# Optimization experiments

Hardware: AMD Instinct MI355X
Metric: run time of the kernel (lower is better)

Reference implementation:

```python
import jax, jax.numpy as jnp
import numpy as np

B, L, D = 2, 2048, 1024
K, M = 32, 4
H = D // K
AH = 4            # anchor heads
DH = K - AH       # decay heads
CK = 4            # conv kernel size
TOTAL = 2 * D + K + K * M


def setup_inputs() -> dict:
    key = jax.random.key(0)
    ks = jax.random.split(key, 7)
    x = jax.random.normal(ks[0], (B, L, D), jnp.float32)
    mask = jnp.ones((B, L), jnp.float32)
    W_in = jax.random.normal(ks[1], (D, TOTAL), jnp.float32) * 0.02
    conv_w = jax.random.normal(ks[2], (CK, TOTAL), jnp.float32) * 0.1  # depthwise taps
    conv_b = jnp.zeros((TOTAL,), jnp.float32)
    grid = np.linspace(-np.pi / 3, np.pi / 3, M).astype(np.float32)
    theta_base = jnp.asarray(np.tile(grid.reshape(1, 1, 1, 1, M), (1, 1, K, 1, 1)))
    theta_resid_scale = jnp.full((K,), 0.1, jnp.float32)
    dr = np.geomspace(0.001, 0.1, DH).astype(np.float32)
    decay_slopes = jnp.asarray(np.log(np.exp(dr) - 1.0).astype(np.float32))
    ar = np.geomspace(0.01, 0.1, AH).astype(np.float32)
    anchor_slopes = jnp.asarray(np.log(np.exp(ar) - 1.0).astype(np.float32))
    score_scale = jnp.ones((K,), jnp.float32)
    norm_scale = jnp.ones((2 * H * M,), jnp.float32)
    gl = float((2.0 / (H * M + H)) ** 0.5)  # glorot std
    W_re = jax.random.normal(ks[3], (H * M, H), jnp.float32) * gl
    W_im = jax.random.normal(ks[4], (H * M, H), jnp.float32) * gl
    W_out = jax.random.normal(ks[5], (D, D), jnp.float32) * 0.02
    return dict(x=x, mask=mask, W_in=W_in, conv_w=conv_w, conv_b=conv_b,
                theta_base=theta_base, theta_resid_scale=theta_resid_scale,
                decay_slopes=decay_slopes, anchor_slopes=anchor_slopes,
                score_scale=score_scale, norm_scale=norm_scale,
                W_re=W_re, W_im=W_im, W_out=W_out)


def _forward(x, mask, W_in, conv_w, conv_b, theta_base, theta_resid_scale,
             decay_slopes, anchor_slopes, score_scale, norm_scale, W_re, W_im, W_out):
    b, l, d = x.shape
    z = x @ W_in  # (b,l,TOTAL)
    # causal depthwise conv, kernel size CK
    zp = jnp.pad(z, ((0, 0), (CK - 1, 0), (0, 0)))
    z = sum(zp[:, t:t + l, :] * conv_w[t] for t in range(CK)) + conv_b

    x_val = z[..., :D].reshape(b, l, K, H)
    x_gate = jax.nn.silu(z[..., D:2 * D])
    s_raw = z[..., 2 * D:2 * D + K].reshape(b, l, K, 1)
    theta_raw = z[..., 2 * D + K:].reshape(b, l, K, M)

    theta_delta = theta_raw / (1.0 + jnp.abs(theta_raw))
    theta_dyn = theta_base + theta_resid_scale.reshape(1, 1, K, 1, 1) * (
        theta_delta.reshape(b, l, K, 1, M) * jnp.float32(np.pi / 3))

    m = mask[:, :, None, None]
    s_raw = s_raw * m
    x_val = x_val * m

    pos = jnp.arange(l, dtype=jnp.float32)
    slopes_d = jax.nn.softplus(decay_slopes).reshape(1, 1, DH, 1)
    dist_d = jnp.maximum(jnp.float32(l - 1) - pos, 0.0)[None, :, None, None]
    w_decay = jnp.exp(-slopes_d * dist_d)
    slopes_a = jax.nn.softplus(anchor_slopes).reshape(1, 1, AH, 1)
    w_anchor = jnp.exp(-slopes_a * pos[None, :, None, None])
    time_weight = jnp.concatenate([w_decay, w_anchor], axis=2)  # (1,l,K,1)

    p = jnp.exp(jnp.clip(score_scale[None, None, :, None] * s_raw, -20.0, 20.0))
    p = p * m

    phi = x_val[..., None] * theta_dyn  # (b,l,K,H,M)
    cos_b = jnp.cos(phi)
    sin_b = jnp.sin(phi)
    p_w = (p * time_weight)[..., None]  # (b,l,K,1,1)

    flat = (b, l, K * H * M)
    merged = jnp.concatenate([
        (p_w * cos_b).reshape(flat),
        (p_w * sin_b).reshape(flat),
        jnp.broadcast_to(p_w, (b, l, K, H, M)).reshape(flat)], axis=-1)
    cs = jnp.cumsum(merged, axis=1)
    num_re, num_im, den = jnp.split(cs, 3, axis=-1)
    inv_den = 1.0 / jnp.maximum(den, jnp.float32(1e-4))
    re = (num_re * inv_den).reshape(b, l, K, H * M)
    im = (num_im * inv_den).reshape(b, l, K, H * M)

    mean_sq = (jnp.sum(re * re, axis=-1) + jnp.sum(im * im, axis=-1)) * (1.0 / (2.0 * H * M))
    rsq = jax.lax.rsqrt(mean_sq[..., None] + 1e-5)
    y = (re * rsq * norm_scale[:H * M]) @ W_re + (im * rsq * norm_scale[H * M:]) @ W_im  # (b,l,K,H)
    y = y.reshape(b, l, D)
    return (y * x_gate) @ W_out


def reference(x, mask, W_in, conv_w, conv_b, theta_base, theta_resid_scale,
              decay_slopes, anchor_slopes, score_scale, norm_scale, W_re, W_im, W_out):
    return _forward(x, mask, W_in, conv_w, conv_b, theta_base, theta_resid_scale,
                    decay_slopes, anchor_slopes, score_scale, norm_scale, W_re, W_im, W_out)
```

## Files before the change

### kernel.cpp

```cpp
#include <hip/hip_runtime.h>
#include <hip/hip_bf16.h>
#include <math.h>

#define B_ 2
#define L_ 2048
#define D_ 1024
#define K_ 32
#define M_ 4
#define H_ 32
#define AH_ 4
#define DH_ 28
#define CK_ 4
#define TOTAL_ 2208
#define NPAD_ 2304
#define BL_ (B_*L_)
#define CL_ 16
#define NC_ (L_/CL_)
#define CTS_ 280
#define ZS_ 72

typedef __attribute__((ext_vector_type(8))) short bf16x8;
typedef __attribute__((ext_vector_type(4))) float f32x4;

static __device__ inline unsigned short f2bu(float f) {
    union { __hip_bfloat16 h; unsigned short u; } cv;
    cv.h = __float2bfloat16(f);
    return cv.u;
}
static __device__ inline float b2f(unsigned short u) {
    union { unsigned short u; __hip_bfloat16 h; } cv;
    cv.u = u;
    return __bfloat162float(cv.h);
}

__global__ void convert_x(const float4* __restrict__ src, ushort* __restrict__ dst) {
    int i = blockIdx.x * 256 + threadIdx.x;
    float4 v = src[i];
    ushort4 o;
    o.x = f2bu(v.x); o.y = f2bu(v.y); o.z = f2bu(v.z); o.w = f2bu(v.w);
    *(ushort4*)(dst + (size_t)i * 4) = o;
}

__global__ void transpose_bf16_pad(const float* __restrict__ src, ushort* __restrict__ dst,
                                   int K, int N) {
    __shared__ float tile[64][65];
    int n0 = blockIdx.x * 64, k0 = blockIdx.y * 64;
    int t = threadIdx.x;
#pragma unroll
    for (int i = 0; i < 16; ++i) {
        int idx = t + i * 256;
        int r = idx >> 6, c = idx & 63;
        int gn = n0 + c;
        tile[r][c] = (gn < N) ? src[(size_t)(k0 + r) * N + gn] : 0.f;
    }
    __syncthreads();
#pragma unroll
    for (int i = 0; i < 16; ++i) {
        int idx = t + i * 256;
        int r = idx >> 6, c = idx & 63;
        dst[(size_t)(n0 + r) * K + k0 + c] = f2bu(tile[c][r]);
    }
}

__global__ void prep_w2(const float* __restrict__ Wre, const float* __restrict__ Wim,
                        const float* __restrict__ nscale, ushort* __restrict__ W2B) {
    int ch = threadIdx.x;
    float ns = nscale[ch];
    for (int hout = 0; hout < 32; ++hout) {
        float w = (ch < 128) ? Wre[ch * 32 + hout] : Wim[(ch - 128) * 32 + hout];
        W2B[hout * 256 + ch] = f2bu(ns * w);
    }
}

__global__ __launch_bounds__(256) void gemm_bt(const ushort* __restrict__ A,
                                               const ushort* __restrict__ Bt,
                                               float* __restrict__ C,
                                               int Kd, int ldc) {
    __shared__ __align__(16) ushort As[128 * 32];
    __shared__ __align__(16) ushort Bs[128 * 32];
    int tid = threadIdx.x;
    int wave = tid >> 6, lane = tid & 63;
    int quad = lane >> 4, l16 = lane & 15;
    int m0 = blockIdx.y * 128, n0 = blockIdx.x * 128;
    int wm = (wave >> 1) * 64, wn = (wave & 1) * 64;
    f32x4 acc[4][4];
#pragma unroll
    for (int i = 0; i < 4; ++i)
#pragma unroll
        for (int j = 0; j < 4; ++j) acc[i][j] = (f32x4){0.f, 0.f, 0.f, 0.f};

    int swzq = quad ^ (l16 & 3);

    for (int k0 = 0; k0 < Kd; k0 += 32) {
#pragma unroll
        for (int i = 0; i < 2; ++i) {
            int s = i * 256 + tid;
            int row = s >> 2;
            int qg = (s & 3) ^ (row & 3);
            const ushort* ga = A + (size_t)(m0 + row) * Kd + k0 + qg * 8;
            const ushort* gb = Bt + (size_t)(n0 + row) * Kd + k0 + qg * 8;
            __builtin_amdgcn_global_load_lds((const __attribute__((address_space(1))) void*)ga,
                                             (__attribute__((address_space(3))) void*)(As + (size_t)s * 8),
                                             16, 0, 0);
            __builtin_amdgcn_global_load_lds((const __attribute__((address_space(1))) void*)gb,
                                             (__attribute__((address_space(3))) void*)(Bs + (size_t)s * 8),
                                             16, 0, 0);
        }
        __syncthreads();
        bf16x8 af[4], bfr[4];
#pragma unroll
        for (int mi = 0; mi < 4; ++mi)
            af[mi] = *(const bf16x8*)(As + (size_t)(wm + mi * 16 + l16) * 32 + swzq * 8);
#pragma unroll
        for (int ni = 0; ni < 4; ++ni)
            bfr[ni] = *(const bf16x8*)(Bs + (size_t)(wn + ni * 16 + l16) * 32 + swzq * 8);
#pragma unroll
        for (int mi = 0; mi < 4; ++mi)
#pragma unroll
            for (int ni = 0; ni < 4; ++ni)
                acc[mi][ni] = __builtin_amdgcn_mfma_f32_16x16x32_bf16(af[mi], bfr[ni], acc[mi][ni], 0, 0, 0);
        __syncthreads();
    }
#pragma unroll
    for (int mi = 0; mi < 4; ++mi)
#pragma unroll
        for (int ni = 0; ni < 4; ++ni)
#pragma unroll
            for (int r = 0; r < 4; ++r) {
                int gm = m0 + wm + mi * 16 + quad * 4 + r;
                int gn = n0 + wn + ni * 16 + l16;
                C[(size_t)gm * ldc + gn] = acc[mi][ni][r];
            }
}

__global__ void conv_kernel(const float* __restrict__ z, const float* __restrict__ cw,
                            const float* __restrict__ cb, float* __restrict__ zck) {
    int t = blockIdx.x * 256 + threadIdx.x;
    if (t >= BL_ * (TOTAL_ / 4)) return;
    int c4 = (t % (TOTAL_ / 4)) * 4;
    int bl = t / (TOTAL_ / 4);
    int l = bl % L_, b = bl / L_;
    float4 acc = *(const float4*)(cb + c4);
#pragma unroll
    for (int tap = 0; tap < CK_; ++tap) {
        int ls = l - (CK_ - 1) + tap;
        if (ls >= 0) {
            float4 zv = *(const float4*)(z + (size_t)(bl - (CK_ - 1) + tap) * NPAD_ + c4);
            float4 wv = *(const float4*)(cw + tap * TOTAL_ + c4);
            acc.x = fmaf(zv.x, wv.x, acc.x);
            acc.y = fmaf(zv.y, wv.y, acc.y);
            acc.z = fmaf(zv.z, wv.z, acc.z);
            acc.w = fmaf(zv.w, wv.w, acc.w);
        }
    }
    if (c4 < D_) {
        int k = c4 >> 5, slot = c4 & 31;
        *(float4*)(zck + ((size_t)(b * K_ + k) * L_ + l) * ZS_ + slot) = acc;
    } else if (c4 < 2 * D_) {
        int cc = c4 - D_;
        int k = cc >> 5, slot = 32 + (cc & 31);
        *(float4*)(zck + ((size_t)(b * K_ + k) * L_ + l) * ZS_ + slot) = acc;
    } else if (c4 < 2 * D_ + K_) {
        float av[4] = {acc.x, acc.y, acc.z, acc.w};
#pragma unroll
        for (int q = 0; q < 4; ++q) {
            int k = c4 + q - 2 * D_;
            zck[((size_t)(b * K_ + k) * L_ + l) * ZS_ + 64] = av[q];
        }
    } else {
        int j = c4 - (2 * D_ + K_);
        int k = j >> 2;
        *(float4*)(zck + ((size_t)(b * K_ + k) * L_ + l) * ZS_ + 68) = acc;
    }
}

__global__ __launch_bounds__(128) void pass1(const float* __restrict__ zck,
                                             const float* __restrict__ mask,
                                             const float* __restrict__ theta_base,
                                             const float* __restrict__ trs_,
                                             const float* __restrict__ dslopes,
                                             const float* __restrict__ aslopes,
                                             const float* __restrict__ sscale_,
                                             const ushort* __restrict__ W2B,
                                             float* __restrict__ cs_re,
                                             float* __restrict__ cs_im,
                                             float* __restrict__ cs_den,
                                             float* __restrict__ vc) {
    __shared__ __align__(16) ushort ct[CL_ * CTS_];
    int nc = blockIdx.x, k = blockIdx.y, b = blockIdx.z;
    int hm = threadIdx.x;
    int h = hm >> 2, m = hm & 3;
    int bk = b * K_ + k;
    size_t bkL = (size_t)bk * L_;
    float raw = (k < DH_) ? dslopes[k] : aslopes[k - DH_];
    float slope = log1pf(__expf(raw));
    float sscale = sscale_[k];
    float trsv = trs_[k];
    float tb = theta_base[k * M_ + m];
    const float PI3 = 1.04719755119659775f;
    float are = 0.f, aim = 0.f, aden = 0.f;
    int l0 = nc * CL_;
#pragma unroll 4
    for (int i = 0; i < CL_; ++i) {
        int l = l0 + i;
        const float* zrow = zck + (bkL + l) * ZS_;
        float mval = mask[b * L_ + l];
        float s_raw = zrow[64] * mval;
        float tr = zrow[68 + m];
        float xv = zrow[h] * mval;
        float arg = fminf(fmaxf(sscale * s_raw, -20.f), 20.f);
        float p = __expf(arg) * mval;
        float tw = (k < DH_) ? __expf(-slope * (float)(L_ - 1 - l)) : __expf(-slope * (float)l);
        float pw = p * tw;
        float td = tr / (1.f + fabsf(tr));
        float theta = tb + trsv * (td * PI3);
        float phi = xv * theta;
        float sv = __sinf(phi), cv = __cosf(phi);
        unsigned short cu_re = f2bu(pw * cv);
        unsigned short cu_im = f2bu(pw * sv);
        are += b2f(cu_re); aim += b2f(cu_im); aden += pw;
        ct[i * CTS_ + hm] = cu_re;
        ct[i * CTS_ + 128 + hm] = cu_im;
    }
    size_t o = ((size_t)(bk * NC_ + nc)) * 128 + hm;
    cs_re[o] = are;
    cs_im[o] = aim;
    if (hm == 0) cs_den[bk * NC_ + nc] = aden;
    __syncthreads();
    int wave = hm >> 6, lane = hm & 63;
    int quad = lane >> 4, l16 = lane & 15;
    f32x4 acc = (f32x4){0.f, 0.f, 0.f, 0.f};
#pragma unroll
    for (int ks = 0; ks < 8; ++ks) {
        bf16x8 af = *(const bf16x8*)(ct + (size_t)l16 * CTS_ + ks * 32 + quad * 8);
        bf16x8 bfr = *(const bf16x8*)(W2B + (size_t)(wave * 16 + l16) * 256 + ks * 32 + quad * 8);
        acc = __builtin_amdgcn_mfma_f32_16x16x32_bf16(af, bfr, acc, 0, 0, 0);
    }
    size_t vbase = (bkL + l0) * 32;
#pragma unroll
    for (int r = 0; r < 4; ++r) {
        int row = quad * 4 + r;
        vc[vbase + (size_t)row * 32 + wave * 16 + l16] = acc[r];
    }
}

__global__ void pass2(float* cs_re, float* cs_im, float* cs_den) {
    int seq = blockIdx.x * 256 + threadIdx.x;
    if (seq >= B_ * K_ * 257) return;
    int bk = seq / 257;
    int ch = seq % 257;
    float* base;
    int stride;
    if (ch < 128) { base = cs_re + (size_t)bk * NC_ * 128 + ch; stride = 128; }
    else if (ch < 256) { base = cs_im + (size_t)bk * NC_ * 128 + (ch - 128); stride = 128; }
    else { base = cs_den + (size_t)bk * NC_; stride = 1; }
    float run = 0.f;
#pragma unroll 4
    for (int i = 0; i < NC_; ++i) {
        float v = base[(size_t)i * stride];
        base[(size_t)i * stride] = run;
        run += v;
    }
}

__global__ __launch_bounds__(64) void scan_kernel(const float* __restrict__ zck,
                                                  const float* __restrict__ mask,
                                                  const float* __restrict__ theta_base,
                                                  const float* __restrict__ trs_,
                                                  const float* __restrict__ dslopes,
                                                  const float* __restrict__ aslopes,
                                                  const float* __restrict__ sscale_,
                                                  const ushort* __restrict__ W2B,
                                                  const float* __restrict__ cs_re,
                                                  const float* __restrict__ cs_im,
                                                  const float* __restrict__ cs_den,
                                                  const float* __restrict__ vc,
                                                  ushort* __restrict__ gq) {
    int nc = blockIdx.x, k = blockIdx.y, b = blockIdx.z;
    int lane = threadIdx.x;
    int bk = b * K_ + k;
    size_t bkL = (size_t)bk * L_;
    int h0 = lane >> 2, h1 = 16 + (lane >> 2), m = lane & 3;
    int hout = lane & 31, half = lane >> 5;
    float raw = (k < DH_) ? dslopes[k] : aslopes[k - DH_];
    float slope = log1pf(__expf(raw));
    float sscale = sscale_[k];
    float trsv = trs_[k];
    float tb = theta_base[k * M_ + m];
    const float PI3 = 1.04719755119659775f;

    size_t o = ((size_t)(bk * NC_ + nc)) * 128;
    const float* srcp = half ? (cs_im + o) : (cs_re + o);
    float u = 0.f;
#pragma unroll 8
    for (int i = 0; i < 128; ++i)
        u = fmaf(srcp[i], b2f(W2B[hout * 256 + half * 128 + i]), u);
    u += __shfl_xor(u, 32, 64);

    float are0 = cs_re[o + lane];
    float are1 = cs_re[o + 64 + lane];
    float aim0 = cs_im[o + lane];
    float aim1 = cs_im[o + 64 + lane];
    float den = cs_den[bk * NC_ + nc];
    int l0 = nc * CL_;

#pragma unroll 4
    for (int i = 0; i < CL_; ++i) {
        int l = l0 + i;
        const float* zrow = zck + (bkL + l) * ZS_;
        float mval = mask[b * L_ + l];
        float s_raw = zrow[64] * mval;
        float tr = zrow[68 + m];
        float xv0 = zrow[h0] * mval;
        float xv1 = zrow[h1] * mval;
        float arg = fminf(fmaxf(sscale * s_raw, -20.f), 20.f);
        float p = __expf(arg) * mval;
        float tw = (k < DH_) ? __expf(-slope * (float)(L_ - 1 - l)) : __expf(-slope * (float)l);
        float pw = p * tw;
        float td = tr / (1.f + fabsf(tr));
        float theta = tb + trsv * (td * PI3);
        float s0 = __sinf(xv0 * theta), c0 = __cosf(xv0 * theta);
        float s1 = __sinf(xv1 * theta), c1 = __cosf(xv1 * theta);
        float cre0 = b2f(f2bu(pw * c0)), cim0 = b2f(f2bu(pw * s0));
        float cre1 = b2f(f2bu(pw * c1)), cim1 = b2f(f2bu(pw * s1));
        are0 += cre0; aim0 += cim0; are1 += cre1; aim1 += cim1;
        den += pw;
        float s = are0 * are0 + are1 * are1 + aim0 * aim0 + aim1 * aim1;
#pragma unroll
        for (int off = 32; off; off >>= 1) s += __shfl_xor(s, off, 64);
        float inv = 1.f / fmaxf(den, 1e-4f);
        float rsq = rsqrtf(inv * inv * s * (1.0f / 256.0f) + 1e-5f);
        float scv = inv * rsq;
        u += vc[(bkL + l) * 32 + hout];
        float y = scv * u;
        float zg = zrow[32 + hout];
        float gate = zg / (1.f + __expf(-zg));
        if (lane < 32) gq[(size_t)(b * L_ + l) * D_ + k * H_ + hout] = f2bu(y * gate);
    }
}

extern "C" void kernel_launch(void* const* d_in, const int* in_sizes, int n_in,
                              void* d_out, int out_size, void* d_ws, size_t ws_size,
                              hipStream_t stream) {
    const float* x = (const float*)d_in[0];
    const float* mask = (const float*)d_in[1];
    const float* W_in = (const float*)d_in[2];
    const float* conv_w = (const float*)d_in[3];
    const float* conv_b = (const float*)d_in[4];
    const float* theta_base = (const float*)d_in[5];
    const float* trs = (const float*)d_in[6];
    const float* dsl = (const float*)d_in[7];
    const float* asl = (const float*)d_in[8];
    const float* ssc = (const float*)d_in[9];
    const float* nsc = (const float*)d_in[10];
    const float* Wre = (const float*)d_in[11];
    const float* Wim = (const float*)d_in[12];
    const float* Wout = (const float*)d_in[13];
    float* out = (float*)d_out;

    char* ws = (char*)d_ws;
    float* zck = (float*)(ws);
    float* z      = (float*)(ws + 37748736ULL);
    float* cs_re  = (float*)(ws + 37748736ULL);
    float* cs_im  = (float*)(ws + 41943040ULL);
    float* cs_den = (float*)(ws + 46137344ULL);
    ushort* gq    = (ushort*)(ws + 46170112ULL);
    ushort* x_bf  = (ushort*)(ws + 75497472ULL);
    ushort* Wt_in = (ushort*)(ws + 83886080ULL);
    float* vc     = (float*)(ws + 75497472ULL);
    ushort* Wt_o  = (ushort*)(ws + 92274688ULL);
    ushort* W2B   = (ushort*)(ws + 94371840ULL);

    convert_x<<<4096, 256, 0, stream>>>((const float4*)x, x_bf);
    transpose_bf16_pad<<<dim3(NPAD_ / 64, 16), 256, 0, stream>>>(W_in, Wt_in, 1024, TOTAL_);
    transpose_bf16_pad<<<dim3(16, 16), 256, 0, stream>>>(Wout, Wt_o, 1024, 1024);
    prep_w2<<<1, 256, 0, stream>>>(Wre, Wim, nsc, W2B);
    gemm_bt<<<dim3(NPAD_ / 128, BL_ / 128), 256, 0, stream>>>(x_bf, Wt_in, z, 1024, NPAD_);
    conv_kernel<<<(BL_ * (TOTAL_ / 4) + 255) / 256, 256, 0, stream>>>(z, conv_w, conv_b, zck);
    pass1<<<dim3(NC_, K_, B_), 128, 0, stream>>>(zck, mask, theta_base, trs, dsl, asl, ssc,
                                                 W2B, cs_re, cs_im, cs_den, vc);
    pass2<<<(B_ * K_ * 257 + 255) / 256, 256, 0, stream>>>(cs_re, cs_im, cs_den);
    scan_kernel<<<dim3(NC_, K_, B_), 64, 0, stream>>>(zck, mask, theta_base, trs, dsl, asl, ssc,
                                                      W2B, cs_re, cs_im, cs_den, vc, gq);
    gemm_bt<<<dim3(D_ / 128, BL_ / 128), 256, 0, stream>>>(gq, Wt_o, out, 1024, 1024);
}
```

Baseline: 304.1 us.

## Cache pass1 contributions and scan projected outputs instead of recomputing in scan

Adds a new path, taken when the workspace is large enough. The conv kernel writes per-head rows with the silu gate precomputed in bf16. pass1 stores its bf16 contributions and time-weighted scores, and new kernels build a prefix sum of the projected vc values, so the final scan no longer recomputes sin/cos or runs the MFMA projection per step. This trades recomputation for more global memory traffic and extra kernel launches, and the path only runs if ws_size meets the new threshold.

```diff
diff --git a/kernel.cpp b/kernel.cpp
--- a/kernel.cpp
+++ b/kernel.cpp
@@ -18,6 +18,7 @@
 #define NC_ (L_/CL_)
 #define CTS_ 280
 #define ZS_ 72
+#define ZS2_ 128
 
 typedef __attribute__((ext_vector_type(8))) short bf16x8;
 typedef __attribute__((ext_vector_type(4))) float f32x4;
@@ -132,6 +133,213 @@
                 C[(size_t)gm * ldc + gn] = acc[mi][ni][r];
             }
 }
+
+
+__global__ void conv_fast(const float* __restrict__ z, const float* __restrict__ cw,
+                          const float* __restrict__ cb, float* __restrict__ zck2,
+                          ushort* __restrict__ gateb) {
+    int t = blockIdx.x * 256 + threadIdx.x;
+    if (t >= BL_ * (TOTAL_ / 4)) return;
+    int c4 = (t % (TOTAL_ / 4)) * 4;
+    int bl = t / (TOTAL_ / 4);
+    int l = bl % L_, b = bl / L_;
+    float4 acc = *(const float4*)(cb + c4);
+#pragma unroll
+    for (int tap = 0; tap < CK_; ++tap) {
+        int ls = l - (CK_ - 1) + tap;
+        if (ls >= 0) {
+            float4 zv = *(const float4*)(z + (size_t)(bl - (CK_ - 1) + tap) * NPAD_ + c4);
+            float4 wv = *(const float4*)(cw + tap * TOTAL_ + c4);
+            acc.x = fmaf(zv.x, wv.x, acc.x);
+            acc.y = fmaf(zv.y, wv.y, acc.y);
+            acc.z = fmaf(zv.z, wv.z, acc.z);
+            acc.w = fmaf(zv.w, wv.w, acc.w);
+        }
+    }
+    if (c4 < D_) {
+        int k = c4 >> 5, slot = c4 & 31;
+        *(float4*)(zck2 + ((size_t)(b * K_ + k) * L_ + l) * ZS2_ + slot) = acc;
+    } else if (c4 < 2 * D_) {
+        int cc = c4 - D_;
+        int k = cc >> 5, hh = cc & 31;
+        float av[4] = {acc.x, acc.y, acc.z, acc.w};
+        ushort4 o;
+        unsigned short* op = (unsigned short*)&o;
+#pragma unroll
+        for (int q = 0; q < 4; ++q) {
+            float zg = av[q];
+            op[q] = f2bu(zg / (1.f + __expf(-zg)));
+        }
+        *(ushort4*)(gateb + ((size_t)(b * K_ + k) * L_ + l) * 32 + hh) = o;
+    } else if (c4 < 2 * D_ + K_) {
+        float av[4] = {acc.x, acc.y, acc.z, acc.w};
+#pragma unroll
+        for (int q = 0; q < 4; ++q) {
+            int k = c4 + q - 2 * D_;
+            zck2[((size_t)(b * K_ + k) * L_ + l) * ZS2_ + 32] = av[q];
+        }
+    } else {
+        int j = c4 - (2 * D_ + K_);
+        int k = j >> 2;
+        *(float4*)(zck2 + ((size_t)(b * K_ + k) * L_ + l) * ZS2_ + 36) = acc;
+    }
+}
+
+__global__ __launch_bounds__(128) void pass1_fast(const float* zck2,
+                                                  const float* __restrict__ mask,
+                                                  const float* __restrict__ theta_base,
+                                                  const float* __restrict__ trs_,
+                                                  const float* __restrict__ dslopes,
+                                                  const float* __restrict__ aslopes,
+                                                  const float* __restrict__ sscale_,
+                                                  const ushort* __restrict__ W2B,
+                                                  float* __restrict__ cs_re,
+                                                  float* __restrict__ cs_im,
+                                                  float* __restrict__ cs_den,
+                                                  float* __restrict__ vc,
+                                                  ushort* ctb,
+                                                  float* __restrict__ pwb) {
+    __shared__ __align__(16) ushort ct[CL_ * CTS_];
+    int nc = blockIdx.x, k = blockIdx.y, b = blockIdx.z;
+    int hm = threadIdx.x;
+    int h = hm >> 2, m = hm & 3;
+    int bk = b * K_ + k;
+    size_t bkL = (size_t)bk * L_;
+    float raw = (k < DH_) ? dslopes[k] : aslopes[k - DH_];
+    float slope = log1pf(__expf(raw));
+    float sscale = sscale_[k];
+    float trsv = trs_[k];
+    float tb = theta_base[k * M_ + m];
+    const float PI3 = 1.04719755119659775f;
+    float are = 0.f, aim = 0.f, aden = 0.f;
+    int l0 = nc * CL_;
+    float tw = (k < DH_) ? __expf(-slope * (float)(L_ - 1 - l0)) : __expf(-slope * (float)l0);
+    float e_s = (k < DH_) ? __expf(slope) : __expf(-slope);
+#pragma unroll 4
+    for (int i = 0; i < CL_; ++i) {
+        int l = l0 + i;
+        const float* zrow = zck2 + (bkL + l) * ZS2_;
+        float mval = mask[b * L_ + l];
+        float s_raw = zrow[32] * mval;
+        float tr = zrow[36 + m];
+        float xv = zrow[h] * mval;
+        float arg = fminf(fmaxf(sscale * s_raw, -20.f), 20.f);
+        float p = __expf(arg) * mval;
+        float pw = p * tw;
+        float td = tr / (1.f + fabsf(tr));
+        float theta = tb + trsv * (td * PI3);
+        float phi = xv * theta;
+        float sv = __sinf(phi), cv = __cosf(phi);
+        unsigned short cu_re = f2bu(pw * cv);
+        unsigned short cu_im = f2bu(pw * sv);
+        are += b2f(cu_re); aim += b2f(cu_im); aden += pw;
+        ct[i * CTS_ + hm] = cu_re;
+        ct[i * CTS_ + 128 + hm] = cu_im;
+        if (hm == 0) pwb[bkL + l] = pw;
+        tw *= e_s;
+    }
+    size_t o = ((size_t)(bk * NC_ + nc)) * 128 + hm;
+    cs_re[o] = are;
+    cs_im[o] = aim;
+    if (hm == 0) cs_den[bk * NC_ + nc] = aden;
+    __syncthreads();
+    int wave = hm >> 6, lane = hm & 63;
+    int quad = lane >> 4, l16 = lane & 15;
+    f32x4 acc = (f32x4){0.f, 0.f, 0.f, 0.f};
+#pragma unroll
+    for (int ks = 0; ks < 8; ++ks) {
+        bf16x8 af = *(const bf16x8*)(ct + (size_t)l16 * CTS_ + ks * 32 + quad * 8);
+        bf16x8 bfr = *(const bf16x8*)(W2B + (size_t)(wave * 16 + l16) * 256 + ks * 32 + quad * 8);
+        acc = __builtin_amdgcn_mfma_f32_16x16x32_bf16(af, bfr, acc, 0, 0, 0);
+    }
+    size_t vbase = (bkL + l0) * 32;
+#pragma unroll
+    for (int r = 0; r < 4; ++r) {
+        int row = quad * 4 + r;
+        vc[vbase + (size_t)row * 32 + wave * 16 + l16] = acc[r];
+    }
+#pragma unroll
+    for (int t = hm; t < CL_ * 64; t += 128) {
+        int i = t >> 6, ln = t & 63;
+        ushort4 w;
+        w.x = ct[i * CTS_ + ln];
+        w.y = ct[i * CTS_ + 64 + ln];
+        w.z = ct[i * CTS_ + 128 + ln];
+        w.w = ct[i * CTS_ + 192 + ln];
+        *(ushort4*)(ctb + (bkL + l0 + i) * 256 + ln * 4) = w;
+    }
+}
+
+__global__ void ucs_kernel(const float* __restrict__ vc, float* __restrict__ ucs) {
+    int idx = blockIdx.x * 256 + threadIdx.x;
+    int hout = idx & 31;
+    int nc = (idx >> 5) & (NC_ - 1);
+    int bk = idx >> 12;
+    float s = 0.f;
+#pragma unroll
+    for (int j = 0; j < CL_; ++j)
+        s += vc[(((size_t)bk * L_) + nc * CL_ + j) * 32 + hout];
+    ucs[((size_t)bk * NC_ + nc) * 32 + hout] = s;
+}
+
+__global__ void uscan_kernel(const float* __restrict__ ucs, float* __restrict__ u_prev) {
+    int idx = blockIdx.x * 256 + threadIdx.x;
+    if (idx >= 64 * 32) return;
+    int hout = idx & 31;
+    int bk = idx >> 5;
+    float run = 0.f;
+#pragma unroll 8
+    for (int nc = 0; nc < NC_; ++nc) {
+        size_t o = ((size_t)bk * NC_ + nc) * 32 + hout;
+        float v = ucs[o];
+        u_prev[o] = run;
+        run += v;
+    }
+}
+
+__global__ __launch_bounds__(64) void scan_fast(const ushort* __restrict__ ctb,
+                                                const float* __restrict__ pwb,
+                                                const float* __restrict__ cs_re,
+                                                const float* __restrict__ cs_im,
+                                                const float* __restrict__ cs_den,
+                                                const float* __restrict__ u_prev,
+                                                const float* __restrict__ vc,
+                                                const ushort* __restrict__ gateb,
+                                                ushort* __restrict__ gq) {
+    int nc = blockIdx.x, k = blockIdx.y, b = blockIdx.z;
+    int lane = threadIdx.x;
+    int bk = b * K_ + k;
+    size_t bkL = (size_t)bk * L_;
+    int hout = lane & 31;
+
+    size_t o = ((size_t)(bk * NC_ + nc)) * 128;
+    float are0 = cs_re[o + lane];
+    float are1 = cs_re[o + 64 + lane];
+    float aim0 = cs_im[o + lane];
+    float aim1 = cs_im[o + 64 + lane];
+    float den = cs_den[bk * NC_ + nc];
+    float u = u_prev[((size_t)(bk * NC_ + nc)) * 32 + hout];
+    int l0 = nc * CL_;
+
+#pragma unroll 4
+    for (int i = 0; i < CL_; ++i) {
+        int l = l0 + i;
+        ushort4 cb = *(const ushort4*)(ctb + (bkL + l) * 256 + lane * 4);
+        float pw = pwb[bkL + l];
+        are0 += b2f(cb.x); are1 += b2f(cb.y);
+        aim0 += b2f(cb.z); aim1 += b2f(cb.w);
+        den += pw;
+        float s = are0 * are0 + are1 * are1 + aim0 * aim0 + aim1 * aim1;
+#pragma unroll
+        for (int off = 32; off; off >>= 1) s += __shfl_xor(s, off, 64);
+        float inv = 1.f / fmaxf(den, 1e-4f);
+        float rsq = rsqrtf(inv * inv * s * (1.0f / 256.0f) + 1e-5f);
+        u += vc[(bkL + l) * 32 + hout];
+        float gv = inv * rsq * u * b2f(gateb[(bkL + l) * 32 + hout]);
+        if (lane < 32) gq[(size_t)(b * L_ + l) * D_ + k * H_ + hout] = f2bu(gv);
+    }
+}
+
 
 __global__ void conv_kernel(const float* __restrict__ z, const float* __restrict__ cw,
                             const float* __restrict__ cb, float* __restrict__ zck) {
@@ -359,28 +567,64 @@
     float* out = (float*)d_out;
 
     char* ws = (char*)d_ws;
-    float* zck = (float*)(ws);
-    float* z      = (float*)(ws + 37748736ULL);
-    float* cs_re  = (float*)(ws + 37748736ULL);
-    float* cs_im  = (float*)(ws + 41943040ULL);
-    float* cs_den = (float*)(ws + 46137344ULL);
-    ushort* gq    = (ushort*)(ws + 46170112ULL);
-    ushort* x_bf  = (ushort*)(ws + 75497472ULL);
-    ushort* Wt_in = (ushort*)(ws + 83886080ULL);
-    float* vc     = (float*)(ws + 75497472ULL);
-    ushort* Wt_o  = (ushort*)(ws + 92274688ULL);
-    ushort* W2B   = (ushort*)(ws + 94371840ULL);
-
-    convert_x<<<4096, 256, 0, stream>>>((const float4*)x, x_bf);
-    transpose_bf16_pad<<<dim3(NPAD_ / 64, 16), 256, 0, stream>>>(W_in, Wt_in, 1024, TOTAL_);
-    transpose_bf16_pad<<<dim3(16, 16), 256, 0, stream>>>(Wout, Wt_o, 1024, 1024);
-    prep_w2<<<1, 256, 0, stream>>>(Wre, Wim, nsc, W2B);
-    gemm_bt<<<dim3(NPAD_ / 128, BL_ / 128), 256, 0, stream>>>(x_bf, Wt_in, z, 1024, NPAD_);
-    conv_kernel<<<(BL_ * (TOTAL_ / 4) + 255) / 256, 256, 0, stream>>>(z, conv_w, conv_b, zck);
-    pass1<<<dim3(NC_, K_, B_), 128, 0, stream>>>(zck, mask, theta_base, trs, dsl, asl, ssc,
-                                                 W2B, cs_re, cs_im, cs_den, vc);
-    pass2<<<(B_ * K_ * 257 + 255) / 256, 256, 0, stream>>>(cs_re, cs_im, cs_den);
-    scan_kernel<<<dim3(NC_, K_, B_), 64, 0, stream>>>(zck, mask, theta_base, trs, dsl, asl, ssc,
-                                                      W2B, cs_re, cs_im, cs_den, vc, gq);
-    gemm_bt<<<dim3(D_ / 128, BL_ / 128), 256, 0, stream>>>(gq, Wt_o, out, 1024, 1024);
-}
+    const size_t NEED_FAST = 115359744ULL;
+
+    if (ws_size >= NEED_FAST) {
+        float* zck2   = (float*)(ws);
+        ushort* ctb   = (ushort*)(ws);
+        ushort* x_bf  = (ushort*)(ws);
+        ushort* Wt_in = (ushort*)(ws + 8388608ULL);
+        ushort* gateb = (ushort*)(ws + 67108864ULL);
+        float* z      = (float*)(ws + 75497472ULL);
+        float* vc     = (float*)(ws + 75497472ULL);
+        float* cs_re  = (float*)(ws + 92274688ULL);
+        float* cs_im  = (float*)(ws + 96468992ULL);
+        float* cs_den = (float*)(ws + 100663296ULL);
+        float* pwb    = (float*)(ws + 100696064ULL);
+        float* u_prev = (float*)(ws + 101220352ULL);
+        float* ucs    = (float*)(ws + 102268928ULL);
+        ushort* gq    = (ushort*)(ws + 103317504ULL);
+        ushort* Wt_o  = (ushort*)(ws + 113246208ULL);
+        ushort* W2B   = (ushort*)(ws + 115343360ULL);
+
+        convert_x<<<4096, 256, 0, stream>>>((const float4*)x, x_bf);
+        transpose_bf16_pad<<<dim3(NPAD_ / 64, 16), 256, 0, stream>>>(W_in, Wt_in, 1024, TOTAL_);
+        transpose_bf16_pad<<<dim3(16, 16), 256, 0, stream>>>(Wout, Wt_o, 1024, 1024);
+        prep_w2<<<1, 256, 0, stream>>>(Wre, Wim, nsc, W2B);
+        gemm_bt<<<dim3(NPAD_ / 128, BL_ / 128), 256, 0, stream>>>(x_bf, Wt_in, z, 1024, NPAD_);
+        conv_fast<<<(BL_ * (TOTAL_ / 4) + 255) / 256, 256, 0, stream>>>(z, conv_w, conv_b, zck2, gateb);
+        pass1_fast<<<dim3(NC_, K_, B_), 128, 0, stream>>>(zck2, mask, theta_base, trs, dsl, asl,
+                                                          ssc, W2B, cs_re, cs_im, cs_den, vc, ctb, pwb);
+        pass2<<<(B_ * K_ * 257 + 255) / 256, 256, 0, stream>>>(cs_re, cs_im, cs_den);
+        ucs_kernel<<<1024, 256, 0, stream>>>(vc, ucs);
+        uscan_kernel<<<8, 256, 0, stream>>>(ucs, u_prev);
+        scan_fast<<<dim3(NC_, K_, B_), 64, 0, stream>>>(ctb, pwb, cs_re, cs_im, cs_den,
+                                                        u_prev, vc, gateb, gq);
+        gemm_bt<<<dim3(D_ / 128, BL_ / 128), 256, 0, stream>>>(gq, Wt_o, out, 1024, 1024);
+    } else {
+        float* zck    = (float*)(ws);
+        float* z      = (float*)(ws + 37748736ULL);
+        float* cs_re  = (float*)(ws + 37748736ULL);
+        float* cs_im  = (float*)(ws + 41943040ULL);
+        float* cs_den = (float*)(ws + 46137344ULL);
+        ushort* gq    = (ushort*)(ws + 46170112ULL);
+        ushort* x_bf  = (ushort*)(ws + 75497472ULL);
+        ushort* Wt_in = (ushort*)(ws + 83886080ULL);
+        float* vc     = (float*)(ws + 75497472ULL);
+        ushort* Wt_o  = (ushort*)(ws + 92274688ULL);
+        ushort* W2B   = (ushort*)(ws + 94371840ULL);
+
+        convert_x<<<4096, 256, 0, stream>>>((const float4*)x, x_bf);
+        transpose_bf16_pad<<<dim3(NPAD_ / 64, 16), 256, 0, stream>>>(W_in, Wt_in, 1024, TOTAL_);
+        transpose_bf16_pad<<<dim3(16, 16), 256, 0, stream>>>(Wout, Wt_o, 1024, 1024);
+        prep_w2<<<1, 256, 0, stream>>>(Wre, Wim, nsc, W2B);
+        gemm_bt<<<dim3(NPAD_ / 128, BL_ / 128), 256, 0, stream>>>(x_bf, Wt_in, z, 1024, NPAD_);
+        conv_kernel<<<(BL_ * (TOTAL_ / 4) + 255) / 256, 256, 0, stream>>>(z, conv_w, conv_b, zck);
+        pass1<<<dim3(NC_, K_, B_), 128, 0, stream>>>(zck, mask, theta_base, trs, dsl, asl, ssc,
+                                                     W2B, cs_re, cs_im, cs_den, vc);
+        pass2<<<(B_ * K_ * 257 + 255) / 256, 256, 0, stream>>>(cs_re, cs_im, cs_den);
+        scan_kernel<<<dim3(NC_, K_, B_), 64, 0, stream>>>(zck, mask, theta_base, trs, dsl, asl, ssc,
+                                                          W2B, cs_re, cs_im, cs_den, vc, gq);
+        gemm_bt<<<dim3(D_ / 128, BL_ / 128), 256, 0, stream>>>(gq, Wt_o, out, 1024, 1024);
+    }
+}
```

After: 301.1 us. No clear change (-1.0%).

## Fuse causal conv into scan passes, merge prep kernels, scan chunk u-offsets

Applied to the files above, without the earlier changes.

Removes the standalone conv kernel and the reshaped zck buffer. The depthwise causal conv is recomputed inside pass1 and the scan kernel from raw z, using register sliding windows. The four prep kernels are merged into one launch. The time-weight exp is replaced by a running multiply. The scan kernel's per-chunk 128-wide dot product for the u offset is replaced by per-chunk partial sums written in pass1 and prefix-scanned in the combined scan2 kernel. This saves a full write and read of the intermediate and several launches, at the cost of strided uncoalesced z reads (row stride NPAD) in the scan kernels and some redundant conv work.

```diff
diff --git a/kernel.cpp b/kernel.cpp
--- a/kernel.cpp
+++ b/kernel.cpp
@@ -17,7 +17,6 @@
 #define CL_ 16
 #define NC_ (L_/CL_)
 #define CTS_ 280
-#define ZS_ 72
 
 typedef __attribute__((ext_vector_type(8))) short bf16x8;
 typedef __attribute__((ext_vector_type(4))) float f32x4;
@@ -32,20 +31,49 @@
     cv.u = u;
     return __bfloat162float(cv.h);
 }
-
-__global__ void convert_x(const float4* __restrict__ src, ushort* __restrict__ dst) {
-    int i = blockIdx.x * 256 + threadIdx.x;
-    float4 v = src[i];
-    ushort4 o;
-    o.x = f2bu(v.x); o.y = f2bu(v.y); o.z = f2bu(v.z); o.w = f2bu(v.w);
-    *(ushort4*)(dst + (size_t)i * 4) = o;
-}
-
-__global__ void transpose_bf16_pad(const float* __restrict__ src, ushort* __restrict__ dst,
-                                   int K, int N) {
+static __device__ inline float conv4(float bias, const float w[4], float r0, float r1,
+                                     float r2, float zc) {
+    return fmaf(w[3], zc, fmaf(w[2], r2, fmaf(w[1], r1, fmaf(w[0], r0, bias))));
+}
+
+__global__ __launch_bounds__(256) void prep_all(const float* __restrict__ x,
+                                                const float* __restrict__ W_in,
+                                                const float* __restrict__ Wout,
+                                                const float* __restrict__ Wre,
+                                                const float* __restrict__ Wim,
+                                                const float* __restrict__ nscale,
+                                                ushort* __restrict__ x_bf,
+                                                ushort* __restrict__ Wt_in,
+                                                ushort* __restrict__ Wt_o,
+                                                ushort* __restrict__ W2B) {
     __shared__ float tile[64][65];
-    int n0 = blockIdx.x * 64, k0 = blockIdx.y * 64;
-    int t = threadIdx.x;
+    int bid = blockIdx.x, t = threadIdx.x;
+    if (bid < 4096) {
+        int i = bid * 256 + t;
+        float4 v = ((const float4*)x)[i];
+        ushort4 o;
+        o.x = f2bu(v.x); o.y = f2bu(v.y); o.z = f2bu(v.z); o.w = f2bu(v.w);
+        *(ushort4*)(x_bf + (size_t)i * 4) = o;
+        return;
+    }
+    const float* src; ushort* dst; int Kd, N, n0, k0;
+    if (bid < 4096 + 576) {
+        int bb = bid - 4096;
+        src = W_in; dst = Wt_in; Kd = 1024; N = TOTAL_;
+        n0 = (bb % 36) * 64; k0 = (bb / 36) * 64;
+    } else if (bid < 4096 + 576 + 256) {
+        int bb = bid - 4096 - 576;
+        src = Wout; dst = Wt_o; Kd = 1024; N = 1024;
+        n0 = (bb % 16) * 64; k0 = (bb / 16) * 64;
+    } else {
+        int ch = t;
+        float ns = nscale[ch];
+        for (int ho = 0; ho < 32; ++ho) {
+            float w = (ch < 128) ? Wre[ch * 32 + ho] : Wim[(ch - 128) * 32 + ho];
+            W2B[ho * 256 + ch] = f2bu(ns * w);
+        }
+        return;
+    }
 #pragma unroll
     for (int i = 0; i < 16; ++i) {
         int idx = t + i * 256;
@@ -58,17 +86,7 @@
     for (int i = 0; i < 16; ++i) {
         int idx = t + i * 256;
         int r = idx >> 6, c = idx & 63;
-        dst[(size_t)(n0 + r) * K + k0 + c] = f2bu(tile[c][r]);
-    }
-}
-
-__global__ void prep_w2(const float* __restrict__ Wre, const float* __restrict__ Wim,
-                        const float* __restrict__ nscale, ushort* __restrict__ W2B) {
-    int ch = threadIdx.x;
-    float ns = nscale[ch];
-    for (int hout = 0; hout < 32; ++hout) {
-        float w = (ch < 128) ? Wre[ch * 32 + hout] : Wim[(ch - 128) * 32 + hout];
-        W2B[hout * 256 + ch] = f2bu(ns * w);
+        dst[(size_t)(n0 + r) * Kd + k0 + c] = f2bu(tile[c][r]);
     }
 }
 
@@ -133,85 +151,70 @@
             }
 }
 
-__global__ void conv_kernel(const float* __restrict__ z, const float* __restrict__ cw,
-                            const float* __restrict__ cb, float* __restrict__ zck) {
-    int t = blockIdx.x * 256 + threadIdx.x;
-    if (t >= BL_ * (TOTAL_ / 4)) return;
-    int c4 = (t % (TOTAL_ / 4)) * 4;
-    int bl = t / (TOTAL_ / 4);
-    int l = bl % L_, b = bl / L_;
-    float4 acc = *(const float4*)(cb + c4);
-#pragma unroll
-    for (int tap = 0; tap < CK_; ++tap) {
-        int ls = l - (CK_ - 1) + tap;
-        if (ls >= 0) {
-            float4 zv = *(const float4*)(z + (size_t)(bl - (CK_ - 1) + tap) * NPAD_ + c4);
-            float4 wv = *(const float4*)(cw + tap * TOTAL_ + c4);
-            acc.x = fmaf(zv.x, wv.x, acc.x);
-            acc.y = fmaf(zv.y, wv.y, acc.y);
-            acc.z = fmaf(zv.z, wv.z, acc.z);
-            acc.w = fmaf(zv.w, wv.w, acc.w);
-        }
-    }
-    if (c4 < D_) {
-        int k = c4 >> 5, slot = c4 & 31;
-        *(float4*)(zck + ((size_t)(b * K_ + k) * L_ + l) * ZS_ + slot) = acc;
-    } else if (c4 < 2 * D_) {
-        int cc = c4 - D_;
-        int k = cc >> 5, slot = 32 + (cc & 31);
-        *(float4*)(zck + ((size_t)(b * K_ + k) * L_ + l) * ZS_ + slot) = acc;
-    } else if (c4 < 2 * D_ + K_) {
-        float av[4] = {acc.x, acc.y, acc.z, acc.w};
-#pragma unroll
-        for (int q = 0; q < 4; ++q) {
-            int k = c4 + q - 2 * D_;
-            zck[((size_t)(b * K_ + k) * L_ + l) * ZS_ + 64] = av[q];
-        }
-    } else {
-        int j = c4 - (2 * D_ + K_);
-        int k = j >> 2;
-        *(float4*)(zck + ((size_t)(b * K_ + k) * L_ + l) * ZS_ + 68) = acc;
-    }
-}
-
-__global__ __launch_bounds__(128) void pass1(const float* __restrict__ zck,
-                                             const float* __restrict__ mask,
-                                             const float* __restrict__ theta_base,
-                                             const float* __restrict__ trs_,
-                                             const float* __restrict__ dslopes,
-                                             const float* __restrict__ aslopes,
-                                             const float* __restrict__ sscale_,
-                                             const ushort* __restrict__ W2B,
-                                             float* __restrict__ cs_re,
-                                             float* __restrict__ cs_im,
-                                             float* __restrict__ cs_den,
-                                             float* __restrict__ vc) {
+__global__ __launch_bounds__(128) void pass1f(const float* __restrict__ z,
+                                              const float* __restrict__ mask,
+                                              const float* __restrict__ theta_base,
+                                              const float* __restrict__ trs_,
+                                              const float* __restrict__ dslopes,
+                                              const float* __restrict__ aslopes,
+                                              const float* __restrict__ sscale_,
+                                              const float* __restrict__ conv_w,
+                                              const float* __restrict__ conv_b,
+                                              const ushort* __restrict__ W2B,
+                                              float* __restrict__ cs_re,
+                                              float* __restrict__ cs_im,
+                                              float* __restrict__ cs_den,
+                                              float* __restrict__ vc,
+                                              float* __restrict__ ucs) {
     __shared__ __align__(16) ushort ct[CL_ * CTS_];
     int nc = blockIdx.x, k = blockIdx.y, b = blockIdx.z;
     int hm = threadIdx.x;
     int h = hm >> 2, m = hm & 3;
     int bk = b * K_ + k;
     size_t bkL = (size_t)bk * L_;
+    int cxv = k * H_ + h, csc = 2 * D_ + k, cth = 2 * D_ + K_ + k * M_ + m;
+    float wx[4], ws4[4], wt4[4];
+#pragma unroll
+    for (int t = 0; t < 4; ++t) {
+        wx[t] = conv_w[t * TOTAL_ + cxv];
+        ws4[t] = conv_w[t * TOTAL_ + csc];
+        wt4[t] = conv_w[t * TOTAL_ + cth];
+    }
+    float bx = conv_b[cxv], bs = conv_b[csc], bt = conv_b[cth];
+    int l0 = nc * CL_;
+    float rx[3], rs[3], rt[3];
+#pragma unroll
+    for (int j = 0; j < 3; ++j) {
+        int ls = l0 - 3 + j;
+        if (ls >= 0) {
+            size_t zo = (size_t)(b * L_ + ls) * NPAD_;
+            rx[j] = z[zo + cxv]; rs[j] = z[zo + csc]; rt[j] = z[zo + cth];
+        } else { rx[j] = 0.f; rs[j] = 0.f; rt[j] = 0.f; }
+    }
     float raw = (k < DH_) ? dslopes[k] : aslopes[k - DH_];
     float slope = log1pf(__expf(raw));
-    float sscale = sscale_[k];
-    float trsv = trs_[k];
-    float tb = theta_base[k * M_ + m];
+    float sscale = sscale_[k], trsv = trs_[k], tb = theta_base[k * M_ + m];
     const float PI3 = 1.04719755119659775f;
+    float tw = (k < DH_) ? __expf(-slope * (float)(L_ - 1 - l0)) : __expf(-slope * (float)l0);
+    float e_s = (k < DH_) ? __expf(slope) : __expf(-slope);
     float are = 0.f, aim = 0.f, aden = 0.f;
-    int l0 = nc * CL_;
 #pragma unroll 4
     for (int i = 0; i < CL_; ++i) {
         int l = l0 + i;
-        const float* zrow = zck + (bkL + l) * ZS_;
-        float mval = mask[b * L_ + l];
-        float s_raw = zrow[64] * mval;
-        float tr = zrow[68 + m];
-        float xv = zrow[h] * mval;
+        int row = b * L_ + l;
+        size_t zo = (size_t)row * NPAD_;
+        float zx = z[zo + cxv], zs = z[zo + csc], zt = z[zo + cth];
+        float mval = mask[row];
+        float xv = conv4(bx, wx, rx[0], rx[1], rx[2], zx) * mval;
+        float s_raw = conv4(bs, ws4, rs[0], rs[1], rs[2], zs) * mval;
+        float tr = conv4(bt, wt4, rt[0], rt[1], rt[2], zt);
+        rx[0] = rx[1]; rx[1] = rx[2]; rx[2] = zx;
+        rs[0] = rs[1]; rs[1] = rs[2]; rs[2] = zs;
+        rt[0] = rt[1]; rt[1] = rt[2]; rt[2] = zt;
         float arg = fminf(fmaxf(sscale * s_raw, -20.f), 20.f);
         float p = __expf(arg) * mval;
-        float tw = (k < DH_) ? __expf(-slope * (float)(L_ - 1 - l)) : __expf(-slope * (float)l);
         float pw = p * tw;
+        tw *= e_s;
         float td = tr / (1.f + fabsf(tr));
         float theta = tb + trsv * (td * PI3);
         float phi = xv * theta;
@@ -239,90 +242,137 @@
     size_t vbase = (bkL + l0) * 32;
 #pragma unroll
     for (int r = 0; r < 4; ++r) {
-        int row = quad * 4 + r;
-        vc[vbase + (size_t)row * 32 + wave * 16 + l16] = acc[r];
-    }
-}
-
-__global__ void pass2(float* cs_re, float* cs_im, float* cs_den) {
-    int seq = blockIdx.x * 256 + threadIdx.x;
-    if (seq >= B_ * K_ * 257) return;
-    int bk = seq / 257;
-    int ch = seq % 257;
-    float* base;
-    int stride;
-    if (ch < 128) { base = cs_re + (size_t)bk * NC_ * 128 + ch; stride = 128; }
-    else if (ch < 256) { base = cs_im + (size_t)bk * NC_ * 128 + (ch - 128); stride = 128; }
-    else { base = cs_den + (size_t)bk * NC_; stride = 1; }
-    float run = 0.f;
+        int rowv = quad * 4 + r;
+        vc[vbase + (size_t)rowv * 32 + wave * 16 + l16] = acc[r];
+    }
+    float part = acc[0] + acc[1] + acc[2] + acc[3];
+    part += __shfl_xor(part, 16, 64);
+    part += __shfl_xor(part, 32, 64);
+    if (quad == 0) ucs[((size_t)(bk * NC_ + nc)) * 32 + wave * 16 + l16] = part;
+}
+
+__global__ void scan2(float* cs_re, float* cs_im, float* cs_den,
+                      const float* __restrict__ ucs, float* __restrict__ u_prev) {
+    int bid = blockIdx.x, tid = threadIdx.x;
+    if (bid < 65) {
+        int seq = bid * 256 + tid;
+        if (seq >= B_ * K_ * 257) return;
+        int bk = seq / 257;
+        int ch = seq % 257;
+        float* base;
+        int stride;
+        if (ch < 128) { base = cs_re + (size_t)bk * NC_ * 128 + ch; stride = 128; }
+        else if (ch < 256) { base = cs_im + (size_t)bk * NC_ * 128 + (ch - 128); stride = 128; }
+        else { base = cs_den + (size_t)bk * NC_; stride = 1; }
+        float run = 0.f;
 #pragma unroll 4
-    for (int i = 0; i < NC_; ++i) {
-        float v = base[(size_t)i * stride];
-        base[(size_t)i * stride] = run;
-        run += v;
-    }
-}
-
-__global__ __launch_bounds__(64) void scan_kernel(const float* __restrict__ zck,
-                                                  const float* __restrict__ mask,
-                                                  const float* __restrict__ theta_base,
-                                                  const float* __restrict__ trs_,
-                                                  const float* __restrict__ dslopes,
-                                                  const float* __restrict__ aslopes,
-                                                  const float* __restrict__ sscale_,
-                                                  const ushort* __restrict__ W2B,
-                                                  const float* __restrict__ cs_re,
-                                                  const float* __restrict__ cs_im,
-                                                  const float* __restrict__ cs_den,
-                                                  const float* __restrict__ vc,
-                                                  ushort* __restrict__ gq) {
+        for (int i = 0; i < NC_; ++i) {
+            float v = base[(size_t)i * stride];
+            base[(size_t)i * stride] = run;
+            run += v;
+        }
+    } else {
+        int idx = (bid - 65) * 256 + tid;
+        int hout = idx & 31;
+        int bk = idx >> 5;
+        float run = 0.f;
+#pragma unroll 8
+        for (int nc = 0; nc < NC_; ++nc) {
+            size_t o = ((size_t)bk * NC_ + nc) * 32 + hout;
+            float v = ucs[o];
+            u_prev[o] = run;
+            run += v;
+        }
+    }
+}
+
+__global__ __launch_bounds__(64) void scan_k7(const float* __restrict__ z,
+                                              const float* __restrict__ mask,
+                                              const float* __restrict__ theta_base,
+                                              const float* __restrict__ trs_,
+                                              const float* __restrict__ dslopes,
+                                              const float* __restrict__ aslopes,
+                                              const float* __restrict__ sscale_,
+                                              const float* __restrict__ conv_w,
+                                              const float* __restrict__ conv_b,
+                                              const float* __restrict__ cs_re,
+                                              const float* __restrict__ cs_im,
+                                              const float* __restrict__ cs_den,
+                                              const float* __restrict__ u_prev,
+                                              const float* __restrict__ vc,
+                                              ushort* __restrict__ gq) {
     int nc = blockIdx.x, k = blockIdx.y, b = blockIdx.z;
     int lane = threadIdx.x;
     int bk = b * K_ + k;
     size_t bkL = (size_t)bk * L_;
-    int h0 = lane >> 2, h1 = 16 + (lane >> 2), m = lane & 3;
-    int hout = lane & 31, half = lane >> 5;
+    int h0 = lane >> 2, m = lane & 3;
+    int hout = lane & 31;
+    int c0 = k * H_ + h0, c1 = k * H_ + 16 + h0;
+    int csc = 2 * D_ + k, cth = 2 * D_ + K_ + k * M_ + m, cg = D_ + k * H_ + hout;
+    float w0[4], w1[4], ws4[4], wt4[4], wg[4];
+#pragma unroll
+    for (int t = 0; t < 4; ++t) {
+        w0[t] = conv_w[t * TOTAL_ + c0];
+        w1[t] = conv_w[t * TOTAL_ + c1];
+        ws4[t] = conv_w[t * TOTAL_ + csc];
+        wt4[t] = conv_w[t * TOTAL_ + cth];
+        wg[t] = conv_w[t * TOTAL_ + cg];
+    }
+    float b0c = conv_b[c0], b1c = conv_b[c1], bsc = conv_b[csc], btc = conv_b[cth], bgc = conv_b[cg];
+    int l0 = nc * CL_;
+    float r0[3], r1[3], rs[3], rt[3], rg[3];
+#pragma unroll
+    for (int j = 0; j < 3; ++j) {
+        int ls = l0 - 3 + j;
+        if (ls >= 0) {
+            size_t zo = (size_t)(b * L_ + ls) * NPAD_;
+            r0[j] = z[zo + c0]; r1[j] = z[zo + c1]; rs[j] = z[zo + csc];
+            rt[j] = z[zo + cth]; rg[j] = z[zo + cg];
+        } else { r0[j] = 0.f; r1[j] = 0.f; rs[j] = 0.f; rt[j] = 0.f; rg[j] = 0.f; }
+    }
     float raw = (k < DH_) ? dslopes[k] : aslopes[k - DH_];
     float slope = log1pf(__expf(raw));
-    float sscale = sscale_[k];
-    float trsv = trs_[k];
-    float tb = theta_base[k * M_ + m];
+    float sscale = sscale_[k], trsv = trs_[k], tb = theta_base[k * M_ + m];
     const float PI3 = 1.04719755119659775f;
+    float tw = (k < DH_) ? __expf(-slope * (float)(L_ - 1 - l0)) : __expf(-slope * (float)l0);
+    float e_s = (k < DH_) ? __expf(slope) : __expf(-slope);
 
     size_t o = ((size_t)(bk * NC_ + nc)) * 128;
-    const float* srcp = half ? (cs_im + o) : (cs_re + o);
-    float u = 0.f;
-#pragma unroll 8
-    for (int i = 0; i < 128; ++i)
-        u = fmaf(srcp[i], b2f(W2B[hout * 256 + half * 128 + i]), u);
-    u += __shfl_xor(u, 32, 64);
-
     float are0 = cs_re[o + lane];
     float are1 = cs_re[o + 64 + lane];
     float aim0 = cs_im[o + lane];
     float aim1 = cs_im[o + 64 + lane];
     float den = cs_den[bk * NC_ + nc];
-    int l0 = nc * CL_;
+    float u = u_prev[((size_t)(bk * NC_ + nc)) * 32 + hout];
 
 #pragma unroll 4
     for (int i = 0; i < CL_; ++i) {
         int l = l0 + i;
-        const float* zrow = zck + (bkL + l) * ZS_;
-        float mval = mask[b * L_ + l];
-        float s_raw = zrow[64] * mval;
-        float tr = zrow[68 + m];
-        float xv0 = zrow[h0] * mval;
-        float xv1 = zrow[h1] * mval;
+        int row = b * L_ + l;
+        size_t zo = (size_t)row * NPAD_;
+        float z0 = z[zo + c0], z1 = z[zo + c1], zs = z[zo + csc];
+        float zt = z[zo + cth], zg = z[zo + cg];
+        float mval = mask[row];
+        float xv0 = conv4(b0c, w0, r0[0], r0[1], r0[2], z0) * mval;
+        float xv1 = conv4(b1c, w1, r1[0], r1[1], r1[2], z1) * mval;
+        float s_raw = conv4(bsc, ws4, rs[0], rs[1], rs[2], zs) * mval;
+        float tr = conv4(btc, wt4, rt[0], rt[1], rt[2], zt);
+        float gpre = conv4(bgc, wg, rg[0], rg[1], rg[2], zg);
+        r0[0] = r0[1]; r0[1] = r0[2]; r0[2] = z0;
+        r1[0] = r1[1]; r1[1] = r1[2]; r1[2] = z1;
+        rs[0] = rs[1]; rs[1] = rs[2]; rs[2] = zs;
+        rt[0] = rt[1]; rt[1] = rt[2]; rt[2] = zt;
+        rg[0] = rg[1]; rg[1] = rg[2]; rg[2] = zg;
         float arg = fminf(fmaxf(sscale * s_raw, -20.f), 20.f);
         float p = __expf(arg) * mval;
-        float tw = (k < DH_) ? __expf(-slope * (float)(L_ - 1 - l)) : __expf(-slope * (float)l);
         float pw = p * tw;
+        tw *= e_s;
         float td = tr / (1.f + fabsf(tr));
         float theta = tb + trsv * (td * PI3);
-        float s0 = __sinf(xv0 * theta), c0 = __cosf(xv0 * theta);
-        float s1 = __sinf(xv1 * theta), c1 = __cosf(xv1 * theta);
-        float cre0 = b2f(f2bu(pw * c0)), cim0 = b2f(f2bu(pw * s0));
-        float cre1 = b2f(f2bu(pw * c1)), cim1 = b2f(f2bu(pw * s1));
+        float s0 = __sinf(xv0 * theta), cv0 = __cosf(xv0 * theta);
+        float s1 = __sinf(xv1 * theta), cv1 = __cosf(xv1 * theta);
+        float cre0 = b2f(f2bu(pw * cv0)), cim0 = b2f(f2bu(pw * s0));
+        float cre1 = b2f(f2bu(pw * cv1)), cim1 = b2f(f2bu(pw * s1));
         are0 += cre0; aim0 += cim0; are1 += cre1; aim1 += cim1;
         den += pw;
         float s = are0 * are0 + are1 * are1 + aim0 * aim0 + aim1 * aim1;
@@ -333,9 +383,8 @@
         float scv = inv * rsq;
         u += vc[(bkL + l) * 32 + hout];
         float y = scv * u;
-        float zg = zrow[32 + hout];
-        float gate = zg / (1.f + __expf(-zg));
-        if (lane < 32) gq[(size_t)(b * L_ + l) * D_ + k * H_ + hout] = f2bu(y * gate);
+        float gate = gpre / (1.f + __expf(-gpre));
+        if (lane < 32) gq[(size_t)row * D_ + k * H_ + hout] = f2bu(y * gate);
     }
 }
 
@@ -359,28 +408,28 @@
     float* out = (float*)d_out;
 
     char* ws = (char*)d_ws;
-    float* zck = (float*)(ws);
-    float* z      = (float*)(ws + 37748736ULL);
-    float* cs_re  = (float*)(ws + 37748736ULL);
-    float* cs_im  = (float*)(ws + 41943040ULL);
-    float* cs_den = (float*)(ws + 46137344ULL);
-    ushort* gq    = (ushort*)(ws + 46170112ULL);
-    ushort* x_bf  = (ushort*)(ws + 75497472ULL);
-    ushort* Wt_in = (ushort*)(ws + 83886080ULL);
-    float* vc     = (float*)(ws + 75497472ULL);
-    ushort* Wt_o  = (ushort*)(ws + 92274688ULL);
-    ushort* W2B   = (ushort*)(ws + 94371840ULL);
-
-    convert_x<<<4096, 256, 0, stream>>>((const float4*)x, x_bf);
-    transpose_bf16_pad<<<dim3(NPAD_ / 64, 16), 256, 0, stream>>>(W_in, Wt_in, 1024, TOTAL_);
-    transpose_bf16_pad<<<dim3(16, 16), 256, 0, stream>>>(Wout, Wt_o, 1024, 1024);
-    prep_w2<<<1, 256, 0, stream>>>(Wre, Wim, nsc, W2B);
+    float* z      = (float*)(ws);
+    ushort* x_bf  = (ushort*)(ws + 37748736ULL);
+    ushort* Wt_in = (ushort*)(ws + 46137344ULL);
+    ushort* Wt_o  = (ushort*)(ws + 50855936ULL);
+    ushort* W2B   = (ushort*)(ws + 52953088ULL);
+    float* vc     = (float*)(ws + 52969472ULL);
+    float* cs_re  = (float*)(ws + 69746688ULL);
+    float* cs_im  = (float*)(ws + 73940992ULL);
+    float* cs_den = (float*)(ws + 78135296ULL);
+    float* ucs    = (float*)(ws + 78168064ULL);
+    float* u_prev = (float*)(ws + 79216640ULL);
+    ushort* gq    = (ushort*)(ws + 80265216ULL);
+
+    prep_all<<<4096 + 576 + 256 + 1, 256, 0, stream>>>(x, W_in, Wout, Wre, Wim, nsc,
+                                                       x_bf, Wt_in, Wt_o, W2B);
     gemm_bt<<<dim3(NPAD_ / 128, BL_ / 128), 256, 0, stream>>>(x_bf, Wt_in, z, 1024, NPAD_);
-    conv_kernel<<<(BL_ * (TOTAL_ / 4) + 255) / 256, 256, 0, stream>>>(z, conv_w, conv_b, zck);
-    pass1<<<dim3(NC_, K_, B_), 128, 0, stream>>>(zck, mask, theta_base, trs, dsl, asl, ssc,
-                                                 W2B, cs_re, cs_im, cs_den, vc);
-    pass2<<<(B_ * K_ * 257 + 255) / 256, 256, 0, stream>>>(cs_re, cs_im, cs_den);
-    scan_kernel<<<dim3(NC_, K_, B_), 64, 0, stream>>>(zck, mask, theta_base, trs, dsl, asl, ssc,
-                                                      W2B, cs_re, cs_im, cs_den, vc, gq);
+    pass1f<<<dim3(NC_, K_, B_), 128, 0, stream>>>(z, mask, theta_base, trs, dsl, asl, ssc,
+                                                  conv_w, conv_b, W2B,
+                                                  cs_re, cs_im, cs_den, vc, ucs);
+    scan2<<<73, 256, 0, stream>>>(cs_re, cs_im, cs_den, ucs, u_prev);
+    scan_k7<<<dim3(NC_, K_, B_), 64, 0, stream>>>(z, mask, theta_base, trs, dsl, asl, ssc,
+                                                  conv_w, conv_b, cs_re, cs_im, cs_den,
+                                                  u_prev, vc, gq);
     gemm_bt<<<dim3(D_ / 128, BL_ / 128), 256, 0, stream>>>(gq, Wt_o, out, 1024, 1024);
 }
```

After: 260.0 us. -14.5%, faster.
